# Performance work log

Measured on AMD Instinct MI355X. Metric: run time of the kernel, lower is better.

## Reference

```python
import jax, jax.numpy as jnp
import numpy as np


def setup_inputs() -> dict:
    key = jax.random.key(0)
    k0, k1, k2, k3, k4, k5 = jax.random.split(key, 6)
    L1, L2, B, D = 512, 512, 32, 1024
    inputs1 = jax.random.normal(k0, (L1, B, D), dtype=jnp.float32)
    inputs2 = jax.random.normal(k1, (L2, B, D), dtype=jnp.float32)
    # mask value 0 marks a valid token (module keeps pairs where both masks == 0)
    mask1 = jax.random.randint(k2, (L1, B), 0, 2, dtype=jnp.int64)
    mask2 = jax.random.randint(k3, (L2, B), 0, 2, dtype=jnp.int64)
    W = jax.random.normal(k4, (D, D), dtype=jnp.float32) * 0.02
    b = jax.random.normal(k5, (1,), dtype=jnp.float32) * 0.02
    return {"inputs1": inputs1, "inputs2": inputs2, "mask1": mask1,
            "mask2": mask2, "W": W, "b": b, "k": 256}


def reference(inputs1, inputs2, mask1, mask2, W, b, k):
    # inputs: [len, bsz, hdim]; masks: [len, bsz]
    H1 = jnp.transpose(inputs1, (1, 0, 2))  # [B, L1, D]
    H2 = jnp.transpose(inputs2, (1, 0, 2))  # [B, L2, D]
    # bilinear scores: H1 @ W @ H2^T + b, then relu  -> [B, L1, L2]
    S = jax.nn.relu(jnp.einsum('bid,de,bje->bij', H1, W, H2) + b[0])
    # pair is valid iff both mask entries are 0
    valid = (mask1.T[:, :, None] == 0) & (mask2.T[:, None, :] == 0)  # [B, L1, L2]
    B = S.shape[0]
    S_flat = jnp.where(valid.reshape(B, -1), S.reshape(B, -1), -jnp.inf)
    num_elems = S_flat.shape[1]
    k_actual = min(k, num_elems)
    q, _ = jax.lax.top_k(S_flat, k_actual)  # [B, k_actual]
    # replace -inf tail entries with the last finite value in each row
    neg = jnp.isneginf(q)
    q_num_finite = k_actual - neg.sum(axis=-1)  # [B]
    fill = jnp.take_along_axis(q, (q_num_finite - 1)[:, None], axis=1)  # [B, 1]
    q = jnp.where(neg, fill, q)
    if k_actual < k:
        q = jnp.concatenate(
            [q, jnp.broadcast_to(q[:, -1:], (B, k - k_actual))], axis=1)
    return q
```

## Files before the change

kernel.cpp:

```cpp
#include <hip/hip_runtime.h>

typedef __bf16 bf16_t;
typedef bf16_t bf16x8 __attribute__((ext_vector_type(8)));
typedef float floatx4 __attribute__((ext_vector_type(4)));

#define L1C 512
#define L2C 512
#define BC  32
#define DC  1024
#define KTOP 256
#define NBIN 4096
#define CAP  512
#define NT   64
#define FBUF 16384

__device__ __forceinline__ unsigned short f2bf(float f) {
    unsigned u = __float_as_uint(f);
    u += 0x7FFFu + ((u >> 16) & 1u);
    return (unsigned short)(u >> 16);
}

__device__ __forceinline__ void g2l16(const unsigned short* g, unsigned short* l) {
    __builtin_amdgcn_global_load_lds((const unsigned int*)g, (unsigned int*)l,
                                     16, 0, 0);
}

__device__ __forceinline__ float decode_key(unsigned k) {
    return __uint_as_float(k & 0x7FFFFFFFu);
}

__global__ __launch_bounds__(512) void scan_kernel(
    const int* __restrict__ mask1, const int* __restrict__ mask2,
    int* __restrict__ idx1, int* __restrict__ idx2,
    unsigned* __restrict__ nv1, unsigned* __restrict__ nv2,
    unsigned* __restrict__ cnt) {
    __shared__ unsigned sc[512];
    int b = blockIdx.x, t = threadIdx.x;
    for (int which = 0; which < 2; which++) {
        const int* m = which ? mask2 : mask1;
        int* idx = which ? idx2 : idx1;
        unsigned v = (m[t * BC + b] == 0) ? 1u : 0u;
        sc[t] = v;
        __syncthreads();
        for (int off = 1; off < 512; off <<= 1) {
            unsigned x = (t >= off) ? sc[t - off] : 0u;
            __syncthreads();
            sc[t] += x;
            __syncthreads();
        }
        if (v) idx[b * 512 + sc[t] - 1] = t;
        if (t == 511) { if (which) nv2[b] = sc[511]; else nv1[b] = sc[511]; }
        __syncthreads();
    }
    if (t < NT) cnt[b * NT + t] = 0;
}

__global__ __launch_bounds__(256) void prep_kernel(
    const float* __restrict__ in1, const float* __restrict__ in2,
    const float* __restrict__ W,
    const int* __restrict__ idx1, const int* __restrict__ idx2,
    const unsigned* __restrict__ nv1, const unsigned* __restrict__ nv2,
    unsigned short* __restrict__ A1c, unsigned short* __restrict__ A2c,
    unsigned short* __restrict__ Wb) {
    int r = blockIdx.x, t = threadIdx.x;
    const float* src;
    unsigned short* dst;
    if (r < 2 * 16384) {
        int which = r >> 14;
        int rr = r & 16383;
        int b = rr >> 9, vi = rr & 511;
        unsigned nv = which ? nv2[b] : nv1[b];
        unsigned pad = (nv + 63u) & ~63u;
        if ((unsigned)vi >= pad) return;
        dst = (which ? A2c : A1c) + ((size_t)b * 512 + vi) * DC;
        if ((unsigned)vi < nv) {
            int l = (which ? idx2 : idx1)[b * 512 + vi];
            src = (which ? in2 : in1) + (size_t)(l * BC + b) * DC;
        } else {
            ushort4 z = {0, 0, 0, 0};
            reinterpret_cast<ushort4*>(dst)[t] = z;
            return;
        }
    } else {
        int r3 = r - 2 * 16384;
        src = W + (size_t)r3 * DC;
        dst = Wb + (size_t)r3 * DC;
    }
    float4 v = reinterpret_cast<const float4*>(src)[t];
    ushort4 o;
    o.x = f2bf(v.x); o.y = f2bf(v.y); o.z = f2bf(v.z); o.w = f2bf(v.w);
    reinterpret_cast<ushort4*>(dst)[t] = o;
}

__global__ __launch_bounds__(256) void gemm1_kernel(
    const unsigned short* __restrict__ A,
    const unsigned short* __restrict__ Bt,
    unsigned short* __restrict__ C,
    const unsigned* __restrict__ nv2) {
    int bi = blockIdx.x >> 3, mt = blockIdx.x & 7;
    unsigned pad2 = (nv2[bi] + 63u) & ~63u;
    if ((unsigned)(mt * 64) >= pad2) return;
    __shared__ unsigned short As[64][32];
    __shared__ unsigned short Bs[128][32];
    int tid = threadIdx.x;
    int wave = tid >> 6, lane = tid & 63;
    int lane15 = lane & 15, quad = lane >> 4;
    size_t m0 = (size_t)bi * 512 + mt * 64;
    size_t n0 = (size_t)blockIdx.y * 128;

    floatx4 zero = {0.f, 0.f, 0.f, 0.f};
    floatx4 acc[4][2];
#pragma unroll
    for (int i = 0; i < 4; i++)
#pragma unroll
        for (int j = 0; j < 2; j++) acc[i][j] = zero;

    for (int k0 = 0; k0 < DC; k0 += 32) {
        {
            int row = tid >> 2, col8 = (tid & 3) * 8;
            g2l16(&A[(m0 + row) * DC + k0 + col8],
                  &As[0][0] + (wave * 64) * 8);
        }
#pragma unroll
        for (int c = 0; c < 2; c++) {
            int cid2 = c * 256 + tid;
            int row = cid2 >> 2, col8 = (cid2 & 3) * 8;
            g2l16(&Bt[(n0 + row) * DC + k0 + col8],
                  &Bs[0][0] + (c * 256 + wave * 64) * 8);
        }
        __syncthreads();
        bf16x8 af[4], bfr[2];
#pragma unroll
        for (int mi = 0; mi < 4; mi++)
            af[mi] = *reinterpret_cast<const bf16x8*>(&As[mi * 16 + lane15][quad * 8]);
#pragma unroll
        for (int ni = 0; ni < 2; ni++)
            bfr[ni] = *reinterpret_cast<const bf16x8*>(
                &Bs[wave * 32 + ni * 16 + lane15][quad * 8]);
#pragma unroll
        for (int mi = 0; mi < 4; mi++)
#pragma unroll
            for (int ni = 0; ni < 2; ni++)
                acc[mi][ni] = __builtin_amdgcn_mfma_f32_16x16x32_bf16(
                    af[mi], bfr[ni], acc[mi][ni], 0, 0, 0);
        __syncthreads();
    }
#pragma unroll
    for (int mi = 0; mi < 4; mi++)
#pragma unroll
        for (int ni = 0; ni < 2; ni++)
#pragma unroll
            for (int r = 0; r < 4; r++) {
                size_t row = m0 + mi * 16 + quad * 4 + r;
                size_t col = n0 + wave * 32 + ni * 16 + lane15;
                C[row * DC + col] = f2bf(acc[mi][ni][r]);
            }
}

__global__ __launch_bounds__(256) void gemm2_kernel(
    const unsigned short* __restrict__ A1c,
    const unsigned short* __restrict__ V,
    const unsigned* __restrict__ nv1, const unsigned* __restrict__ nv2,
    const float* __restrict__ bptr,
    unsigned* __restrict__ cand,
    unsigned* __restrict__ cnt) {
    int L = blockIdx.x;
    int xcd = L & 7, tile = (L >> 3) & 63, chunk = L >> 9;
    int b = xcd + (chunk << 3);
    int tx = tile & 7, ty = tile >> 3;
    int m0 = ty * 64, n0 = tx * 64;
    int gblk = b * NT + tile;
    int tid = threadIdx.x;
    unsigned nv1v = nv1[b], nv2v = nv2[b];
    unsigned pad1 = (nv1v + 63u) & ~63u, pad2 = (nv2v + 63u) & ~63u;
    if ((unsigned)m0 >= pad1 || (unsigned)n0 >= pad2) {
        if (tid == 0) cnt[gblk] = 0;
        return;
    }
    __shared__ unsigned short As[64][32];
    __shared__ unsigned short Bs[64][32];
    __shared__ unsigned lh[NBIN];
    __shared__ unsigned csum[256];
    __shared__ unsigned sel_c, sel_a, tsh, lcnt, zeq;
    int wave = tid >> 6, lane = tid & 63;
    int lane15 = lane & 15, quad = lane >> 4;
    const unsigned short* Ab = A1c + (size_t)b * 512 * DC;
    const unsigned short* Bb = V + (size_t)b * 512 * DC;

    for (int i = tid; i < NBIN; i += 256) lh[i] = 0;
    if (tid == 0) { sel_c = 0xFFFFFFFFu; lcnt = 0; zeq = 0; }

    floatx4 zero = {0.f, 0.f, 0.f, 0.f};
    floatx4 acc[4];
#pragma unroll
    for (int i = 0; i < 4; i++) acc[i] = zero;

    for (int k0 = 0; k0 < DC; k0 += 32) {
        int row = tid >> 2, col8 = (tid & 3) * 8;
        g2l16(&Ab[(size_t)(m0 + row) * DC + k0 + col8],
              &As[0][0] + (wave * 64) * 8);
        g2l16(&Bb[(size_t)(n0 + row) * DC + k0 + col8],
              &Bs[0][0] + (wave * 64) * 8);
        __syncthreads();
        bf16x8 af, bfr[4];
        af = *reinterpret_cast<const bf16x8*>(&As[wave * 16 + lane15][quad * 8]);
#pragma unroll
        for (int ni = 0; ni < 4; ni++)
            bfr[ni] = *reinterpret_cast<const bf16x8*>(&Bs[ni * 16 + lane15][quad * 8]);
#pragma unroll
        for (int ni = 0; ni < 4; ni++)
            acc[ni] = __builtin_amdgcn_mfma_f32_16x16x32_bf16(
                af, bfr[ni], acc[ni], 0, 0, 0);
        __syncthreads();
    }

    float bias = bptr[0];
    unsigned zc = 0;
#pragma unroll
    for (int ni = 0; ni < 4; ni++) {
        int jl = n0 + ni * 16 + lane15;
        int v2 = (unsigned)jl < nv2v;
#pragma unroll
        for (int r = 0; r < 4; r++) {
            int il = m0 + wave * 16 + quad * 4 + r;
            float s = acc[ni][r] + bias;
            if (v2 && (unsigned)il < nv1v) {
                if (s > 0.f)
                    atomicAdd(&lh[(__float_as_uint(s) | 0x80000000u) >> 20], 1u);
                else
                    zc++;
            }
        }
    }
    if (zc) atomicAdd(&lh[2048], zc);
    __syncthreads();
    unsigned s16 = 0;
#pragma unroll
    for (int i = 0; i < 16; i++) s16 += lh[tid * 16 + i];
    csum[tid] = s16;
    __syncthreads();
    for (int off = 1; off < 256; off <<= 1) {
        unsigned v = (tid + off < 256) ? csum[tid + off] : 0u;
        __syncthreads();
        csum[tid] += v;
        __syncthreads();
    }
    {
        unsigned above = (tid < 255) ? csum[tid + 1] : 0u;
        if (tid >= 128 && csum[tid] >= KTOP && above < KTOP) {
            sel_c = (unsigned)tid; sel_a = above;
        }
    }
    __syncthreads();
    if (tid == 0) {
        if (sel_c == 0xFFFFFFFFu) {
            tsh = 2048u << 20;
        } else {
            unsigned cum = sel_a, bin = 2048;
            for (int bb = (int)sel_c * 16 + 15; bb >= (int)sel_c * 16; --bb) {
                unsigned hb = lh[bb];
                if (cum + hb >= KTOP) { bin = (unsigned)bb; break; }
                cum += hb;
            }
            tsh = bin << 20;
        }
    }
    __syncthreads();
    unsigned T = tsh;
    unsigned base = (unsigned)gblk * CAP;
#pragma unroll
    for (int ni = 0; ni < 4; ni++) {
        int jl = n0 + ni * 16 + lane15;
        int v2 = (unsigned)jl < nv2v;
#pragma unroll
        for (int r = 0; r < 4; r++) {
            int il = m0 + wave * 16 + quad * 4 + r;
            float s = acc[ni][r] + bias;
            s = s > 0.f ? s : 0.f;
            unsigned key = (v2 && (unsigned)il < nv1v)
                               ? (__float_as_uint(s) | 0x80000000u) : 0u;
            if (key > T) {
                unsigned p = atomicAdd(&lcnt, 1u);
                if (p < CAP) cand[base + p] = key;
            } else if (key == T) {
                unsigned z = atomicAdd(&zeq, 1u);
                if (z < KTOP) {
                    unsigned p = atomicAdd(&lcnt, 1u);
                    if (p < CAP) cand[base + p] = key;
                }
            }
        }
    }
    __syncthreads();
    if (tid == 0) cnt[gblk] = lcnt < CAP ? lcnt : CAP;
}

__global__ __launch_bounds__(1024) void final_kernel(
    const unsigned* __restrict__ cand, const unsigned* __restrict__ cnt,
    float* __restrict__ out) {
    __shared__ unsigned buf[FBUF];
    __shared__ unsigned h[NBIN];
    __shared__ unsigned ss[256];
    __shared__ unsigned scnt_s[NT], off_s[NT];
    __shared__ unsigned ntot_s, sel_c, sel_a, B_s, R_s, mcount;
    __shared__ int have_s;
    __shared__ unsigned srt[256];
    int b = blockIdx.x, tid = threadIdx.x;
    int wv = tid >> 6, ln = tid & 63;

    if (tid < NT) {
        unsigned c = cnt[b * NT + tid];
        scnt_s[tid] = c < CAP ? c : CAP;
    }
    __syncthreads();
    if (tid == 0) {
        unsigned o = 0;
        for (int i = 0; i < NT; i++) {
            unsigned c = scnt_s[i];
            if (o + c > FBUF) c = (o < FBUF) ? FBUF - o : 0;
            scnt_s[i] = c;
            off_s[i] = o;
            o += c;
        }
        ntot_s = o;
        have_s = 1;
    }
    __syncthreads();
    for (int s = wv; s < NT; s += 16) {
        unsigned c = scnt_s[s], o = off_s[s];
        const unsigned* p = cand + (size_t)(b * NT + s) * CAP;
        for (unsigned i = ln; i < c; i += 64) buf[o + i] = p[i];
    }
    __syncthreads();
    unsigned n = ntot_s;

    unsigned Kr = KTOP;
    unsigned pfx = 0;
    unsigned kth = 0;
    for (int pass = 0; pass < 3; pass++) {
        int bins = (pass < 2) ? NBIN : 256;
        int shift = (pass == 0) ? 20 : (pass == 1) ? 8 : 0;
        int nch = bins >> 4;
        for (int i = tid; i < bins; i += 1024) h[i] = 0;
        __syncthreads();
        for (unsigned i = tid; i < n; i += 1024) {
            unsigned k = buf[i];
            bool ok = (pass == 0) ||
                      (pass == 1 && (k >> 20) == pfx) ||
                      (pass == 2 && (k >> 8) == pfx);
            if (ok) atomicAdd(&h[(k >> shift) & (bins - 1)], 1u);
        }
        __syncthreads();
        if (tid < nch) {
            unsigned s = 0;
#pragma unroll
            for (int i = 0; i < 16; i++) s += h[tid * 16 + i];
            ss[tid] = s;
        }
        __syncthreads();
        for (int off = 1; off < nch; off <<= 1) {
            unsigned v = 0;
            if (tid < nch && tid + (unsigned)off < (unsigned)nch) v = ss[tid + off];
            __syncthreads();
            if (tid < nch) ss[tid] += v;
            __syncthreads();
        }
        if (pass == 0) {
            if (tid == 0) have_s = (ss[0] >= KTOP);
            __syncthreads();
            if (!have_s) break;
        }
        if (tid < nch) {
            unsigned above = (tid + 1 < (unsigned)nch) ? ss[tid + 1] : 0u;
            if (above < Kr && ss[tid] >= Kr) { sel_c = tid; sel_a = above; }
        }
        __syncthreads();
        if (tid == 0) {
            unsigned cum = sel_a;
            for (int bb = (int)sel_c * 16 + 15; bb >= (int)sel_c * 16; --bb) {
                unsigned hb = h[bb];
                if (cum + hb >= Kr) { B_s = (unsigned)bb; R_s = Kr - cum; break; }
                cum += hb;
            }
        }
        __syncthreads();
        unsigned Bv = B_s;
        Kr = R_s;
        if (pass == 0) pfx = Bv;
        else if (pass == 1) pfx = (pfx << 12) | Bv;
        else kth = (pfx << 8) | Bv;
        __syncthreads();
    }

    if (tid == 0) mcount = 0;
    __syncthreads();
    int have = have_s;
    unsigned lim = have ? kth : 0u;
    for (unsigned i = tid; i < n; i += 1024) {
        unsigned k = buf[i];
        if (k > lim) {
            unsigned p = atomicAdd(&mcount, 1u);
            if (p < 256) srt[p] = k;
        }
    }
    __syncthreads();
    unsigned m = mcount;
    if (tid < 256 && tid >= (int)m) srt[tid] = have ? kth : 0u;
    for (int k2 = 2; k2 <= 256; k2 <<= 1) {
        for (int j2 = k2 >> 1; j2 > 0; j2 >>= 1) {
            __syncthreads();
            if (tid < 256) {
                int ixj = tid ^ j2;
                if (ixj > tid) {
                    unsigned a = srt[tid], c = srt[ixj];
                    bool up = (tid & k2) == 0;
                    if (up ? (a < c) : (a > c)) { srt[tid] = c; srt[ixj] = a; }
                }
            }
        }
    }
    __syncthreads();
    if (tid < 256) {
        unsigned nval = have ? KTOP : (m < KTOP ? m : KTOP);
        float v;
        if ((unsigned)tid < nval) v = decode_key(srt[tid]);
        else v = (nval > 0) ? decode_key(srt[nval - 1]) : -__builtin_inff();
        out[b * KTOP + tid] = v;
    }
}

extern "C" void kernel_launch(void* const* d_in, const int* in_sizes, int n_in,
                              void* d_out, int out_size, void* d_ws, size_t ws_size,
                              hipStream_t stream) {
    const float* in1   = (const float*)d_in[0];
    const float* in2   = (const float*)d_in[1];
    const int*   mask1 = (const int*)d_in[2];
    const int*   mask2 = (const int*)d_in[3];
    const float* W     = (const float*)d_in[4];
    const float* bias  = (const float*)d_in[5];
    float* out = (float*)d_out;

    char* ws = (char*)d_ws;
    size_t off = 0;
    const size_t nElem = (size_t)512 * BC * DC;
    unsigned short* A1c = (unsigned short*)(ws + off); off += nElem * 2;
    unsigned short* A2c = (unsigned short*)(ws + off); off += nElem * 2;
    unsigned short* Wb  = (unsigned short*)(ws + off); off += (size_t)DC * DC * 2;
    unsigned short* V   = (unsigned short*)(ws + off); off += nElem * 2;
    unsigned* cand = (unsigned*)(ws + off); off += (size_t)BC * NT * CAP * 4;
    unsigned* cnt  = (unsigned*)(ws + off); off += (size_t)BC * NT * 4;
    int* idx1 = (int*)(ws + off); off += (size_t)BC * 512 * 4;
    int* idx2 = (int*)(ws + off); off += (size_t)BC * 512 * 4;
    unsigned* nv1 = (unsigned*)(ws + off); off += BC * 4;
    unsigned* nv2 = (unsigned*)(ws + off); off += BC * 4;

    scan_kernel<<<BC, 512, 0, stream>>>(mask1, mask2, idx1, idx2, nv1, nv2, cnt);
    prep_kernel<<<2 * 16384 + 1024, 256, 0, stream>>>(
        in1, in2, W, idx1, idx2, nv1, nv2, A1c, A2c, Wb);
    gemm1_kernel<<<dim3(256, 8), 256, 0, stream>>>(A2c, Wb, V, nv2);
    gemm2_kernel<<<2048, 256, 0, stream>>>(A1c, V, nv1, nv2, bias, cand, cnt);
    final_kernel<<<BC, 1024, 0, stream>>>(cand, cnt, out);
}
```

Before: 262.1 us.

## Enlarge gemm1 tiles to 128x128 and double K-step to 64 in both GEMMs

gemm1 now computes 128x128 output tiles with a 2x2 wave layout and 4x4 MFMA accumulators per wave, halving the grid in M. Both GEMMs now load a 64-wide K slab per iteration as two 32-wide halves, which halves the number of barrier pairs per tile. The aim is more operand reuse per LDS load and less synchronisation overhead. The cost is more LDS and registers per block, which may lower occupancy. Padding skips in gemm1 are now coarser at 128 rows, so more padded rows may be computed.

```diff
diff --git a/kernel.cpp b/kernel.cpp
--- a/kernel.cpp
+++ b/kernel.cpp
@@ -97,62 +97,64 @@
     const unsigned short* __restrict__ Bt,
     unsigned short* __restrict__ C,
     const unsigned* __restrict__ nv2) {
-    int bi = blockIdx.x >> 3, mt = blockIdx.x & 7;
+    int bi = blockIdx.x >> 2, mt = blockIdx.x & 3;
     unsigned pad2 = (nv2[bi] + 63u) & ~63u;
-    if ((unsigned)(mt * 64) >= pad2) return;
-    __shared__ unsigned short As[64][32];
-    __shared__ unsigned short Bs[128][32];
+    if ((unsigned)(mt * 128) >= pad2) return;
+    __shared__ unsigned short As[2][128][32];
+    __shared__ unsigned short Bs[2][128][32];
     int tid = threadIdx.x;
     int wave = tid >> 6, lane = tid & 63;
     int lane15 = lane & 15, quad = lane >> 4;
-    size_t m0 = (size_t)bi * 512 + mt * 64;
+    int wm = wave >> 1, wn = wave & 1;
+    size_t m0 = (size_t)bi * 512 + mt * 128;
     size_t n0 = (size_t)blockIdx.y * 128;
 
     floatx4 zero = {0.f, 0.f, 0.f, 0.f};
-    floatx4 acc[4][2];
+    floatx4 acc[4][4];
 #pragma unroll
     for (int i = 0; i < 4; i++)
 #pragma unroll
-        for (int j = 0; j < 2; j++) acc[i][j] = zero;
-
-    for (int k0 = 0; k0 < DC; k0 += 32) {
-        {
-            int row = tid >> 2, col8 = (tid & 3) * 8;
-            g2l16(&A[(m0 + row) * DC + k0 + col8],
-                  &As[0][0] + (wave * 64) * 8);
-        }
-#pragma unroll
-        for (int c = 0; c < 2; c++) {
-            int cid2 = c * 256 + tid;
-            int row = cid2 >> 2, col8 = (cid2 & 3) * 8;
-            g2l16(&Bt[(n0 + row) * DC + k0 + col8],
-                  &Bs[0][0] + (c * 256 + wave * 64) * 8);
-        }
-        __syncthreads();
-        bf16x8 af[4], bfr[2];
-#pragma unroll
-        for (int mi = 0; mi < 4; mi++)
-            af[mi] = *reinterpret_cast<const bf16x8*>(&As[mi * 16 + lane15][quad * 8]);
-#pragma unroll
-        for (int ni = 0; ni < 2; ni++)
-            bfr[ni] = *reinterpret_cast<const bf16x8*>(
-                &Bs[wave * 32 + ni * 16 + lane15][quad * 8]);
-#pragma unroll
-        for (int mi = 0; mi < 4; mi++)
-#pragma unroll
-            for (int ni = 0; ni < 2; ni++)
-                acc[mi][ni] = __builtin_amdgcn_mfma_f32_16x16x32_bf16(
-                    af[mi], bfr[ni], acc[mi][ni], 0, 0, 0);
+        for (int j = 0; j < 4; j++) acc[i][j] = zero;
+
+    for (int k0 = 0; k0 < DC; k0 += 64) {
+#pragma unroll
+        for (int c = 0; c < 4; c++) {
+            int cid = c * 256 + tid;
+            int h = cid >> 9, row = (cid >> 2) & 127, col8 = (cid & 3) * 8;
+            unsigned short* lb = &As[0][0][0] + (c * 256 + wave * 64) * 8;
+            g2l16(&A[(m0 + row) * DC + k0 + h * 32 + col8], lb);
+            unsigned short* lb2 = &Bs[0][0][0] + (c * 256 + wave * 64) * 8;
+            g2l16(&Bt[(n0 + row) * DC + k0 + h * 32 + col8], lb2);
+        }
+        __syncthreads();
+#pragma unroll
+        for (int h = 0; h < 2; h++) {
+            bf16x8 af[4], bfr[4];
+#pragma unroll
+            for (int mi = 0; mi < 4; mi++)
+                af[mi] = *reinterpret_cast<const bf16x8*>(
+                    &As[h][wm * 64 + mi * 16 + lane15][quad * 8]);
+#pragma unroll
+            for (int ni = 0; ni < 4; ni++)
+                bfr[ni] = *reinterpret_cast<const bf16x8*>(
+                    &Bs[h][wn * 64 + ni * 16 + lane15][quad * 8]);
+#pragma unroll
+            for (int mi = 0; mi < 4; mi++)
+#pragma unroll
+                for (int ni = 0; ni < 4; ni++)
+                    acc[mi][ni] = __builtin_amdgcn_mfma_f32_16x16x32_bf16(
+                        af[mi], bfr[ni], acc[mi][ni], 0, 0, 0);
+        }
         __syncthreads();
     }
 #pragma unroll
     for (int mi = 0; mi < 4; mi++)
 #pragma unroll
-        for (int ni = 0; ni < 2; ni++)
+        for (int ni = 0; ni < 4; ni++)
 #pragma unroll
             for (int r = 0; r < 4; r++) {
-                size_t row = m0 + mi * 16 + quad * 4 + r;
-                size_t col = n0 + wave * 32 + ni * 16 + lane15;
+                size_t row = m0 + wm * 64 + mi * 16 + quad * 4 + r;
+                size_t col = n0 + wn * 64 + ni * 16 + lane15;
                 C[row * DC + col] = f2bf(acc[mi][ni][r]);
             }
 }
@@ -177,8 +179,8 @@
         if (tid == 0) cnt[gblk] = 0;
         return;
     }
-    __shared__ unsigned short As[64][32];
-    __shared__ unsigned short Bs[64][32];
+    __shared__ unsigned short As[2][64][32];
+    __shared__ unsigned short Bs[2][64][32];
     __shared__ unsigned lh[NBIN];
     __shared__ unsigned csum[256];
     __shared__ unsigned sel_c, sel_a, tsh, lcnt, zeq;
@@ -195,22 +197,31 @@
 #pragma unroll
     for (int i = 0; i < 4; i++) acc[i] = zero;
 
-    for (int k0 = 0; k0 < DC; k0 += 32) {
-        int row = tid >> 2, col8 = (tid & 3) * 8;
-        g2l16(&Ab[(size_t)(m0 + row) * DC + k0 + col8],
-              &As[0][0] + (wave * 64) * 8);
-        g2l16(&Bb[(size_t)(n0 + row) * DC + k0 + col8],
-              &Bs[0][0] + (wave * 64) * 8);
-        __syncthreads();
-        bf16x8 af, bfr[4];
-        af = *reinterpret_cast<const bf16x8*>(&As[wave * 16 + lane15][quad * 8]);
-#pragma unroll
-        for (int ni = 0; ni < 4; ni++)
-            bfr[ni] = *reinterpret_cast<const bf16x8*>(&Bs[ni * 16 + lane15][quad * 8]);
-#pragma unroll
-        for (int ni = 0; ni < 4; ni++)
-            acc[ni] = __builtin_amdgcn_mfma_f32_16x16x32_bf16(
-                af, bfr[ni], acc[ni], 0, 0, 0);
+    for (int k0 = 0; k0 < DC; k0 += 64) {
+#pragma unroll
+        for (int c = 0; c < 2; c++) {
+            int cid = c * 256 + tid;
+            int h = cid >> 8, row = (cid >> 2) & 63, col8 = (cid & 3) * 8;
+            unsigned short* lb = &As[0][0][0] + (c * 256 + wave * 64) * 8;
+            g2l16(&Ab[(size_t)(m0 + row) * DC + k0 + h * 32 + col8], lb);
+            unsigned short* lb2 = &Bs[0][0][0] + (c * 256 + wave * 64) * 8;
+            g2l16(&Bb[(size_t)(n0 + row) * DC + k0 + h * 32 + col8], lb2);
+        }
+        __syncthreads();
+#pragma unroll
+        for (int h = 0; h < 2; h++) {
+            bf16x8 af, bfr[4];
+            af = *reinterpret_cast<const bf16x8*>(
+                &As[h][wave * 16 + lane15][quad * 8]);
+#pragma unroll
+            for (int ni = 0; ni < 4; ni++)
+                bfr[ni] = *reinterpret_cast<const bf16x8*>(
+                    &Bs[h][ni * 16 + lane15][quad * 8]);
+#pragma unroll
+            for (int ni = 0; ni < 4; ni++)
+                acc[ni] = __builtin_amdgcn_mfma_f32_16x16x32_bf16(
+                    af, bfr[ni], acc[ni], 0, 0, 0);
+        }
         __syncthreads();
     }
 
@@ -457,7 +468,7 @@
     scan_kernel<<<BC, 512, 0, stream>>>(mask1, mask2, idx1, idx2, nv1, nv2, cnt);
     prep_kernel<<<2 * 16384 + 1024, 256, 0, stream>>>(
         in1, in2, W, idx1, idx2, nv1, nv2, A1c, A2c, Wb);
-    gemm1_kernel<<<dim3(256, 8), 256, 0, stream>>>(A2c, Wb, V, nv2);
+    gemm1_kernel<<<dim3(128, 8), 256, 0, stream>>>(A2c, Wb, V, nv2);
     gemm2_kernel<<<2048, 256, 0, stream>>>(A1c, V, nv1, nv2, bias, cand, cnt);
     final_kernel<<<BC, 1024, 0, stream>>>(cand, cnt, out);
 }
```

Result: faster. 248.4 us (-5.2%).
